# Optimization experiments

Measured on AMD Instinct MI355X. Metric: run time of the kernel, lower is better.

## Reference

```python
import jax, jax.numpy as jnp
import numpy as np

H, W = 256, 256          # heat_map_shape
P = 512                  # number of ground-truth points
ALPHA = -5.0             # soft-min exponent


def setup_inputs() -> dict:
    key = jax.random.key(0)
    k1, k2 = jax.random.split(key)
    heat_map = jax.random.uniform(k1, (H, W), dtype=jnp.float32)  # values in [0,1]
    # points in [0,H) x [0,W), float coords (never exactly on grid -> dist > 0)
    points = jax.random.uniform(k2, (P, 2), dtype=jnp.float32) * jnp.array([H, W], jnp.float32)
    return {"heat_map": heat_map, "points": points}


def reference(heat_map, points):
    # grid: (H, W, 2) with torch.meshgrid 'ij' indexing semantics
    ys = jnp.arange(H, dtype=jnp.float32)
    xs = jnp.arange(W, dtype=jnp.float32)
    grid = jnp.stack(jnp.meshgrid(ys, xs, indexing="ij"), axis=-1)

    delta = grid[:, :, None, :] - points[None, None]          # (H, W, P, 2)
    dist = jnp.sqrt(jnp.sum(delta * delta, axis=-1))          # (H, W, P)

    # term 1: heatmap-weighted min distance, normalized by L1 norm of heatmap
    weighted_min = jnp.sum(heat_map * jnp.min(dist, axis=-1)) / jnp.sum(jnp.abs(heat_map))

    # term 2: generalized (power) mean soft-min over spatial dims, then mean over P
    hm = heat_map[..., None]                                  # (H, W, 1)
    weighted_dist = hm * dist + (1.0 - hm) * jnp.max(dist)    # (H, W, P)
    soft_min = jnp.mean(weighted_dist ** ALPHA, axis=(0, 1)) ** (1.0 / ALPHA)  # (P,)
    mean_soft_min = jnp.mean(soft_min)

    return weighted_min + mean_soft_min
```

## Files before the change

### kernel.cpp

```cpp
#include <hip/hip_runtime.h>

#define HH 256
#define WW 256
#define NPIX (HH * WW)
#define NP 512

#define PPB 4
#define SLICE_ROWS 32
#define NSLICES (HH / SLICE_ROWS)
#define NPGRP (NP / PPB)
#define NB_T2 (NPGRP * NSLICES)
#define NB_T1 (NPIX / 256)
#define NB_TOTAL (NB_T1 + NB_T2)

#define WS_SP   0
#define WS_T1A  (NP * NSLICES)
#define WS_T1B  (WS_T1A + NB_T1)

__global__ __launch_bounds__(256) void whd_main(const float* __restrict__ hm,
                                                const float* __restrict__ pts,
                                                float* __restrict__ ws) {
    const int tid = threadIdx.x;
    const int bid = blockIdx.x;
    __shared__ float sred[PPB][4];
    __shared__ float dred[4];

    if (bid < NB_T1) {
        const int idx = bid * 256 + tid;
        const float fi = (float)(idx >> 8);
        const float fj = (float)(idx & (WW - 1));
        const float4* pts4 = (const float4*)pts;
        float m0 = 3.4e38f, m1 = 3.4e38f, m2 = 3.4e38f, m3 = 3.4e38f;
        #pragma unroll 4
        for (int i = 0; i < NP / 2; i += 4) {
            float4 q0 = pts4[i], q1 = pts4[i + 1], q2 = pts4[i + 2], q3 = pts4[i + 3];
            float dy, dx;
            dy = fi - q0.x; dx = fj - q0.y; m0 = fminf(m0, fmaf(dy, dy, dx * dx));
            dy = fi - q0.z; dx = fj - q0.w; m1 = fminf(m1, fmaf(dy, dy, dx * dx));
            dy = fi - q1.x; dx = fj - q1.y; m2 = fminf(m2, fmaf(dy, dy, dx * dx));
            dy = fi - q1.z; dx = fj - q1.w; m3 = fminf(m3, fmaf(dy, dy, dx * dx));
            dy = fi - q2.x; dx = fj - q2.y; m0 = fminf(m0, fmaf(dy, dy, dx * dx));
            dy = fi - q2.z; dx = fj - q2.w; m1 = fminf(m1, fmaf(dy, dy, dx * dx));
            dy = fi - q3.x; dx = fj - q3.y; m2 = fminf(m2, fmaf(dy, dy, dx * dx));
            dy = fi - q3.z; dx = fj - q3.w; m3 = fminf(m3, fmaf(dy, dy, dx * dx));
        }
        float mind = __builtin_amdgcn_sqrtf(fminf(fminf(m0, m1), fminf(m2, m3)));
        float h  = hm[idx];
        float v1 = h * mind;
        float v2 = fabsf(h);
        #pragma unroll
        for (int off = 32; off; off >>= 1) {
            v1 += __shfl_down(v1, off, 64);
            v2 += __shfl_down(v2, off, 64);
        }
        if ((tid & 63) == 0) { sred[0][tid >> 6] = v1; sred[1][tid >> 6] = v2; }
        __syncthreads();
        if (tid == 0) ws[WS_T1A + bid] = sred[0][0] + sred[0][1] + sred[0][2] + sred[0][3];
        if (tid == 1) ws[WS_T1B + bid] = sred[1][0] + sred[1][1] + sred[1][2] + sred[1][3];
    } else {
        const int b2 = bid - NB_T1;
        float m = 0.f;
        #pragma unroll
        for (int t = 0; t < 2; ++t) {
            int p = tid + t * 256;
            float py = pts[2 * p], px = pts[2 * p + 1];
            float my = fmaxf(py * py, (255.f - py) * (255.f - py));
            float mx = fmaxf(px * px, (255.f - px) * (255.f - px));
            m = fmaxf(m, my + mx);
        }
        #pragma unroll
        for (int off = 32; off; off >>= 1) m = fmaxf(m, __shfl_down(m, off, 64));
        if ((tid & 63) == 0) dred[tid >> 6] = m;
        __syncthreads();
        const float dmax = __builtin_amdgcn_sqrtf(
            fmaxf(fmaxf(dred[0], dred[1]), fmaxf(dred[2], dred[3])));

        const int pgrp  = b2 & (NPGRP - 1);
        const int slice = b2 >> 7;
        const int p0    = pgrp * PPB;

        float py[PPB], px[PPB];
        #pragma unroll
        for (int a = 0; a < PPB; ++a) {
            py[a] = pts[2 * (p0 + a)];
            px[a] = pts[2 * (p0 + a) + 1];
        }

        const float col0 = (float)((tid & 63) << 2);
        float dx2[PPB][4];
        #pragma unroll
        for (int a = 0; a < PPB; ++a)
            #pragma unroll
            for (int c = 0; c < 4; ++c) {
                float dx = col0 + (float)c - px[a];
                dx2[a][c] = dx * dx;
            }

        const float4* hm4 = (const float4*)hm;
        const int   gbase   = slice * (SLICE_ROWS * WW / 4) + tid;
        const float rowbase = (float)(slice * SLICE_ROWS + (tid >> 6));
        float acc[PPB] = {0.f, 0.f, 0.f, 0.f};

        #pragma unroll
        for (int k = 0; k < 8; ++k) {
            float4 h4 = hm4[gbase + k * 256];
            const float row = rowbase + (float)(4 * k);
            const float hx[4] = {h4.x, h4.y, h4.z, h4.w};
            float ct[4];
            #pragma unroll
            for (int c = 0; c < 4; ++c) ct[c] = fmaf(-hx[c], dmax, dmax);
            float dy2[PPB];
            #pragma unroll
            for (int a = 0; a < PPB; ++a) { float dy = row - py[a]; dy2[a] = dy * dy; }

            #pragma unroll
            for (int a = 0; a < PPB; ++a) {
                #pragma unroll
                for (int c = 0; c < 4; ++c) {
                    float d  = __builtin_amdgcn_sqrtf(dy2[a] + dx2[a][c]);
                    float w  = fmaf(hx[c], d, ct[c]);
                    float r  = __builtin_amdgcn_rcpf(w);
                    float r2 = r * r;
                    acc[a]   = fmaf(r2 * r2, r, acc[a]);
                }
            }
        }

        #pragma unroll
        for (int a = 0; a < PPB; ++a) {
            float v = acc[a];
            #pragma unroll
            for (int off = 32; off; off >>= 1) v += __shfl_down(v, off, 64);
            if ((tid & 63) == 0) sred[a][tid >> 6] = v;
        }
        __syncthreads();
        if (tid < PPB) {
            ws[WS_SP + (p0 + tid) * NSLICES + slice] =
                sred[tid][0] + sred[tid][1] + sred[tid][2] + sred[tid][3];
        }
    }
}

__global__ __launch_bounds__(NP) void whd_final(const float* __restrict__ ws,
                                                float* __restrict__ out) {
    const int t = threadIdx.x;
    const float4* w4 = (const float4*)(ws + WS_SP);
    float4 a = w4[t * 2], b = w4[t * 2 + 1];
    float S = ((a.x + a.y) + (a.z + a.w)) + ((b.x + b.y) + (b.z + b.w));
    float sm = exp2f(-0.2f * log2f(S * (1.f / (float)NPIX)));
    float v1 = (t < NB_T1) ? ws[WS_T1A + t] : 0.f;
    float v2 = (t < NB_T1) ? ws[WS_T1B + t] : 0.f;

    #pragma unroll
    for (int off = 32; off; off >>= 1) {
        sm += __shfl_down(sm, off, 64);
        v1 += __shfl_down(v1, off, 64);
        v2 += __shfl_down(v2, off, 64);
    }
    __shared__ float red[3][8];
    if ((t & 63) == 0) { int w = t >> 6; red[0][w] = sm; red[1][w] = v1; red[2][w] = v2; }
    __syncthreads();
    if (t == 0) {
        float rsm = 0.f, r1 = 0.f, r2 = 0.f;
        #pragma unroll
        for (int w = 0; w < 8; ++w) { rsm += red[0][w]; r1 += red[1][w]; r2 += red[2][w]; }
        out[0] = r1 / r2 + rsm * (1.f / (float)NP);
    }
}

extern "C" void kernel_launch(void* const* d_in, const int* in_sizes, int n_in,
                              void* d_out, int out_size, void* d_ws, size_t ws_size,
                              hipStream_t stream) {
    const float* hm  = (const float*)d_in[0];
    const float* pts = (const float*)d_in[1];
    float* ws  = (float*)d_ws;
    float* out = (float*)d_out;

    whd_main <<<NB_TOTAL, 256, 0, stream>>>(hm, pts, ws);
    whd_final<<<1,        NP,  0, stream>>>(ws, out);
}
```

Measured before the change: 70.47 us.

## Restructure distance math into float2 pairs for packed FP32 and prefetch heatmap

Rewrites both the min-distance and soft-min inner loops to work on float2 pairs so the compiler can emit packed FP32 (v_pk_fma/v_pk_mul/v_pk_add) instructions on CDNA. It also loads all eight heatmap float4s into registers up front rather than inside the compute loop, and interleaves the wavefront shuffle reductions across the four points. Sqrt and rcp have no packed form, so the transcendental-heavy soft-min path may gain little, and the extra live registers could reduce occupancy.

```diff
diff --git a/kernel.cpp b/kernel.cpp
--- a/kernel.cpp
+++ b/kernel.cpp
@@ -17,6 +17,23 @@
 #define WS_T1A  (NP * NSLICES)
 #define WS_T1B  (WS_T1A + NB_T1)
 
+__device__ __forceinline__ float2 pk2(float a, float b) { return make_float2(a, b); }
+__device__ __forceinline__ float2 pk_add(float2 a, float2 b) { return make_float2(a.x + b.x, a.y + b.y); }
+__device__ __forceinline__ float2 pk_sub(float2 a, float2 b) { return make_float2(a.x - b.x, a.y - b.y); }
+__device__ __forceinline__ float2 pk_mul(float2 a, float2 b) { return make_float2(a.x * b.x, a.y * b.y); }
+__device__ __forceinline__ float2 pk_fma(float2 a, float2 b, float2 c) {
+    return make_float2(fmaf(a.x, b.x, c.x), fmaf(a.y, b.y, c.y));
+}
+__device__ __forceinline__ float2 pk_min(float2 a, float2 b) {
+    return make_float2(fminf(a.x, b.x), fminf(a.y, b.y));
+}
+__device__ __forceinline__ float2 pk_sqrt(float2 a) {
+    return make_float2(__builtin_amdgcn_sqrtf(a.x), __builtin_amdgcn_sqrtf(a.y));
+}
+__device__ __forceinline__ float2 pk_rcp(float2 a) {
+    return make_float2(__builtin_amdgcn_rcpf(a.x), __builtin_amdgcn_rcpf(a.y));
+}
+
 __global__ __launch_bounds__(256) void whd_main(const float* __restrict__ hm,
                                                 const float* __restrict__ pts,
                                                 float* __restrict__ ws) {
@@ -29,22 +46,24 @@
         const int idx = bid * 256 + tid;
         const float fi = (float)(idx >> 8);
         const float fj = (float)(idx & (WW - 1));
+        const float2 fi2 = pk2(fi, fi), fj2 = pk2(fj, fj);
         const float4* pts4 = (const float4*)pts;
-        float m0 = 3.4e38f, m1 = 3.4e38f, m2 = 3.4e38f, m3 = 3.4e38f;
+        float2 ma = pk2(3.4e38f, 3.4e38f), mb = ma, mc = ma, md = ma;
         #pragma unroll 4
         for (int i = 0; i < NP / 2; i += 4) {
             float4 q0 = pts4[i], q1 = pts4[i + 1], q2 = pts4[i + 2], q3 = pts4[i + 3];
-            float dy, dx;
-            dy = fi - q0.x; dx = fj - q0.y; m0 = fminf(m0, fmaf(dy, dy, dx * dx));
-            dy = fi - q0.z; dx = fj - q0.w; m1 = fminf(m1, fmaf(dy, dy, dx * dx));
-            dy = fi - q1.x; dx = fj - q1.y; m2 = fminf(m2, fmaf(dy, dy, dx * dx));
-            dy = fi - q1.z; dx = fj - q1.w; m3 = fminf(m3, fmaf(dy, dy, dx * dx));
-            dy = fi - q2.x; dx = fj - q2.y; m0 = fminf(m0, fmaf(dy, dy, dx * dx));
-            dy = fi - q2.z; dx = fj - q2.w; m1 = fminf(m1, fmaf(dy, dy, dx * dx));
-            dy = fi - q3.x; dx = fj - q3.y; m2 = fminf(m2, fmaf(dy, dy, dx * dx));
-            dy = fi - q3.z; dx = fj - q3.w; m3 = fminf(m3, fmaf(dy, dy, dx * dx));
-        }
-        float mind = __builtin_amdgcn_sqrtf(fminf(fminf(m0, m1), fminf(m2, m3)));
+            float2 dy, dx;
+            dy = pk_sub(fi2, pk2(q0.x, q0.z)); dx = pk_sub(fj2, pk2(q0.y, q0.w));
+            ma = pk_min(ma, pk_fma(dy, dy, pk_mul(dx, dx)));
+            dy = pk_sub(fi2, pk2(q1.x, q1.z)); dx = pk_sub(fj2, pk2(q1.y, q1.w));
+            mb = pk_min(mb, pk_fma(dy, dy, pk_mul(dx, dx)));
+            dy = pk_sub(fi2, pk2(q2.x, q2.z)); dx = pk_sub(fj2, pk2(q2.y, q2.w));
+            mc = pk_min(mc, pk_fma(dy, dy, pk_mul(dx, dx)));
+            dy = pk_sub(fi2, pk2(q3.x, q3.z)); dx = pk_sub(fj2, pk2(q3.y, q3.w));
+            md = pk_min(md, pk_fma(dy, dy, pk_mul(dx, dx)));
+        }
+        float2 mm = pk_min(pk_min(ma, mb), pk_min(mc, md));
+        float mind = __builtin_amdgcn_sqrtf(fminf(mm.x, mm.y));
         float h  = hm[idx];
         float v1 = h * mind;
         float v2 = fabsf(h);
@@ -74,6 +93,7 @@
         __syncthreads();
         const float dmax = __builtin_amdgcn_sqrtf(
             fmaxf(fmaxf(dred[0], dred[1]), fmaxf(dred[2], dred[3])));
+        const float2 dmax2 = pk2(dmax, dmax);
 
         const int pgrp  = b2 & (NPGRP - 1);
         const int slice = b2 >> 7;
@@ -87,51 +107,64 @@
         }
 
         const float col0 = (float)((tid & 63) << 2);
-        float dx2[PPB][4];
-        #pragma unroll
-        for (int a = 0; a < PPB; ++a)
-            #pragma unroll
-            for (int c = 0; c < 4; ++c) {
-                float dx = col0 + (float)c - px[a];
-                dx2[a][c] = dx * dx;
-            }
+        float2 dx2A[PPB], dx2B[PPB];
+        #pragma unroll
+        for (int a = 0; a < PPB; ++a) {
+            float2 dA = pk2(col0 + 0.f - px[a], col0 + 1.f - px[a]);
+            float2 dB = pk2(col0 + 2.f - px[a], col0 + 3.f - px[a]);
+            dx2A[a] = pk_mul(dA, dA);
+            dx2B[a] = pk_mul(dB, dB);
+        }
 
         const float4* hm4 = (const float4*)hm;
         const int   gbase   = slice * (SLICE_ROWS * WW / 4) + tid;
         const float rowbase = (float)(slice * SLICE_ROWS + (tid >> 6));
-        float acc[PPB] = {0.f, 0.f, 0.f, 0.f};
-
+
+        float4 h4s[8];
+        #pragma unroll
+        for (int k = 0; k < 8; ++k) h4s[k] = hm4[gbase + k * 256];
+
+        float2 accA[PPB], accB[PPB];
+        #pragma unroll
+        for (int a = 0; a < PPB; ++a) { accA[a] = pk2(0.f, 0.f); accB[a] = pk2(0.f, 0.f); }
+
+        const float2 one2 = pk2(1.f, 1.f);
         #pragma unroll
         for (int k = 0; k < 8; ++k) {
-            float4 h4 = hm4[gbase + k * 256];
+            const float4 h4 = h4s[k];
             const float row = rowbase + (float)(4 * k);
-            const float hx[4] = {h4.x, h4.y, h4.z, h4.w};
-            float ct[4];
-            #pragma unroll
-            for (int c = 0; c < 4; ++c) ct[c] = fmaf(-hx[c], dmax, dmax);
-            float dy2[PPB];
-            #pragma unroll
-            for (int a = 0; a < PPB; ++a) { float dy = row - py[a]; dy2[a] = dy * dy; }
+            const float2 hA = pk2(h4.x, h4.y), hB = pk2(h4.z, h4.w);
+            const float2 ctA = pk_mul(pk_sub(one2, hA), dmax2);
+            const float2 ctB = pk_mul(pk_sub(one2, hB), dmax2);
 
             #pragma unroll
             for (int a = 0; a < PPB; ++a) {
-                #pragma unroll
-                for (int c = 0; c < 4; ++c) {
-                    float d  = __builtin_amdgcn_sqrtf(dy2[a] + dx2[a][c]);
-                    float w  = fmaf(hx[c], d, ct[c]);
-                    float r  = __builtin_amdgcn_rcpf(w);
-                    float r2 = r * r;
-                    acc[a]   = fmaf(r2 * r2, r, acc[a]);
-                }
+                float dy = row - py[a];
+                float2 dy2 = pk2(dy * dy, dy * dy);
+                float2 dA = pk_sqrt(pk_add(dy2, dx2A[a]));
+                float2 dB = pk_sqrt(pk_add(dy2, dx2B[a]));
+                float2 wA = pk_fma(hA, dA, ctA);
+                float2 wB = pk_fma(hB, dB, ctB);
+                float2 rA = pk_rcp(wA);
+                float2 rB = pk_rcp(wB);
+                float2 r2A = pk_mul(rA, rA), r2B = pk_mul(rB, rB);
+                accA[a] = pk_fma(pk_mul(r2A, r2A), rA, accA[a]);
+                accB[a] = pk_fma(pk_mul(r2B, r2B), rB, accB[a]);
             }
         }
 
-        #pragma unroll
-        for (int a = 0; a < PPB; ++a) {
-            float v = acc[a];
+        float v[PPB];
+        #pragma unroll
+        for (int a = 0; a < PPB; ++a)
+            v[a] = (accA[a].x + accA[a].y) + (accB[a].x + accB[a].y);
+        #pragma unroll
+        for (int off = 32; off; off >>= 1) {
             #pragma unroll
-            for (int off = 32; off; off >>= 1) v += __shfl_down(v, off, 64);
-            if ((tid & 63) == 0) sred[a][tid >> 6] = v;
+            for (int a = 0; a < PPB; ++a) v[a] += __shfl_down(v[a], off, 64);
+        }
+        if ((tid & 63) == 0) {
+            #pragma unroll
+            for (int a = 0; a < PPB; ++a) sred[a][tid >> 6] = v[a];
         }
         __syncthreads();
         if (tid < PPB) {
```

New measurement: 72.45 us. +2.8%, slower.

## Pack soft-min math into f32x2 ops and batch reciprocals across four pixels

Applied to the files above, without the earlier changes.

Rewrites the term-2 inner loop to use packed FP32 instructions (v_pk_add/mul/fma) for pairs of columns. It replaces four per-pixel reciprocals with one shared reciprocal plus product-based reconstruction (Montgomery batch inversion), cutting transcendental-unit work. It also hoists all heatmap loads ahead of the dmax reduction so they overlap, and computes dmax on a single wavefront. The batched inverse risks overflow or underflow of the four-way product and adds multiplies. Inline asm may also limit compiler scheduling.

```diff
diff --git a/kernel.cpp b/kernel.cpp
--- a/kernel.cpp
+++ b/kernel.cpp
@@ -17,13 +17,24 @@
 #define WS_T1A  (NP * NSLICES)
 #define WS_T1B  (WS_T1A + NB_T1)
 
+typedef float f32x2 __attribute__((ext_vector_type(2)));
+__device__ __forceinline__ f32x2 pk_add(f32x2 a, f32x2 b) {
+    f32x2 d; asm("v_pk_add_f32 %0, %1, %2" : "=v"(d) : "v"(a), "v"(b)); return d;
+}
+__device__ __forceinline__ f32x2 pk_mul(f32x2 a, f32x2 b) {
+    f32x2 d; asm("v_pk_mul_f32 %0, %1, %2" : "=v"(d) : "v"(a), "v"(b)); return d;
+}
+__device__ __forceinline__ f32x2 pk_fma(f32x2 a, f32x2 b, f32x2 c) {
+    f32x2 d; asm("v_pk_fma_f32 %0, %1, %2, %3" : "=v"(d) : "v"(a), "v"(b), "v"(c)); return d;
+}
+
 __global__ __launch_bounds__(256) void whd_main(const float* __restrict__ hm,
                                                 const float* __restrict__ pts,
                                                 float* __restrict__ ws) {
     const int tid = threadIdx.x;
     const int bid = blockIdx.x;
     __shared__ float sred[PPB][4];
-    __shared__ float dred[4];
+    __shared__ float dmax_sh;
 
     if (bid < NB_T1) {
         const int idx = bid * 256 + tid;
@@ -58,27 +69,34 @@
         if (tid == 0) ws[WS_T1A + bid] = sred[0][0] + sred[0][1] + sred[0][2] + sred[0][3];
         if (tid == 1) ws[WS_T1B + bid] = sred[1][0] + sred[1][1] + sred[1][2] + sred[1][3];
     } else {
-        const int b2 = bid - NB_T1;
-        float m = 0.f;
-        #pragma unroll
-        for (int t = 0; t < 2; ++t) {
-            int p = tid + t * 256;
-            float py = pts[2 * p], px = pts[2 * p + 1];
-            float my = fmaxf(py * py, (255.f - py) * (255.f - py));
-            float mx = fmaxf(px * px, (255.f - px) * (255.f - px));
-            m = fmaxf(m, my + mx);
-        }
-        #pragma unroll
-        for (int off = 32; off; off >>= 1) m = fmaxf(m, __shfl_down(m, off, 64));
-        if ((tid & 63) == 0) dred[tid >> 6] = m;
-        __syncthreads();
-        const float dmax = __builtin_amdgcn_sqrtf(
-            fmaxf(fmaxf(dred[0], dred[1]), fmaxf(dred[2], dred[3])));
-
+        const int b2    = bid - NB_T1;
         const int pgrp  = b2 & (NPGRP - 1);
         const int slice = b2 >> 7;
         const int p0    = pgrp * PPB;
 
+        const float4* hm4 = (const float4*)hm;
+        const int gbase = slice * (SLICE_ROWS * WW / 4) + tid;
+        float4 h4s[8];
+        #pragma unroll
+        for (int k = 0; k < 8; ++k) h4s[k] = hm4[gbase + k * 256];
+
+        if (tid < 64) {
+            float m = 0.f;
+            #pragma unroll
+            for (int t = 0; t < 8; ++t) {
+                int p = tid + t * 64;
+                float py_ = pts[2 * p], px_ = pts[2 * p + 1];
+                float my = fmaxf(py_ * py_, (255.f - py_) * (255.f - py_));
+                float mx = fmaxf(px_ * px_, (255.f - px_) * (255.f - px_));
+                m = fmaxf(m, my + mx);
+            }
+            #pragma unroll
+            for (int off = 32; off; off >>= 1) m = fmaxf(m, __shfl_down(m, off, 64));
+            if (tid == 0) dmax_sh = __builtin_amdgcn_sqrtf(m);
+        }
+        __syncthreads();
+        const float dmax = dmax_sh;
+
         float py[PPB], px[PPB];
         #pragma unroll
         for (int a = 0; a < PPB; ++a) {
@@ -87,51 +105,73 @@
         }
 
         const float col0 = (float)((tid & 63) << 2);
-        float dx2[PPB][4];
+        f32x2 dx2A[PPB], dx2B[PPB];
+        #pragma unroll
+        for (int a = 0; a < PPB; ++a) {
+            float d0 = col0 + 0.f - px[a], d1 = col0 + 1.f - px[a];
+            float d2 = col0 + 2.f - px[a], d3 = col0 + 3.f - px[a];
+            dx2A[a].x = d0 * d0; dx2A[a].y = d1 * d1;
+            dx2B[a].x = d2 * d2; dx2B[a].y = d3 * d3;
+        }
+
+        const float rowbase = (float)(slice * SLICE_ROWS + (tid >> 6));
+        f32x2 accA[PPB], accB[PPB];
+        #pragma unroll
+        for (int a = 0; a < PPB; ++a) {
+            accA[a].x = 0.f; accA[a].y = 0.f;
+            accB[a].x = 0.f; accB[a].y = 0.f;
+        }
+
+        #pragma unroll
+        for (int k = 0; k < 8; ++k) {
+            const float4 h4 = h4s[k];
+            const float row = rowbase + (float)(4 * k);
+            f32x2 hA;  hA.x = h4.x;  hA.y = h4.y;
+            f32x2 hB;  hB.x = h4.z;  hB.y = h4.w;
+            f32x2 ctA; ctA.x = fmaf(-h4.x, dmax, dmax); ctA.y = fmaf(-h4.y, dmax, dmax);
+            f32x2 ctB; ctB.x = fmaf(-h4.z, dmax, dmax); ctB.y = fmaf(-h4.w, dmax, dmax);
+
+            #pragma unroll
+            for (int a = 0; a < PPB; ++a) {
+                float dy  = row - py[a];
+                float dy2 = dy * dy;
+                f32x2 dy2p; dy2p.x = dy2; dy2p.y = dy2;
+                f32x2 sA = pk_add(dy2p, dx2A[a]);
+                f32x2 sB = pk_add(dy2p, dx2B[a]);
+                f32x2 dA, dB;
+                dA.x = __builtin_amdgcn_sqrtf(sA.x); dA.y = __builtin_amdgcn_sqrtf(sA.y);
+                dB.x = __builtin_amdgcn_sqrtf(sB.x); dB.y = __builtin_amdgcn_sqrtf(sB.y);
+                f32x2 wA = pk_fma(hA, dA, ctA);
+                f32x2 wB = pk_fma(hB, dB, ctB);
+                float p1 = wA.x * wA.y;
+                float p2 = p1 * wB.x;
+                float p3 = p2 * wB.y;
+                float r  = __builtin_amdgcn_rcpf(p3);
+                float i3 = r * p2;
+                float q  = r * wB.y;
+                float i2 = q * p1;
+                float q2 = q * wB.x;
+                f32x2 iA; iA.x = q2 * wA.y; iA.y = q2 * wA.x;
+                f32x2 iB; iB.x = i2;        iB.y = i3;
+                f32x2 tA = pk_mul(iA, iA);
+                f32x2 tB = pk_mul(iB, iB);
+                accA[a] = pk_fma(pk_mul(tA, tA), iA, accA[a]);
+                accB[a] = pk_fma(pk_mul(tB, tB), iB, accB[a]);
+            }
+        }
+
+        float v[PPB];
         #pragma unroll
         for (int a = 0; a < PPB; ++a)
-            #pragma unroll
-            for (int c = 0; c < 4; ++c) {
-                float dx = col0 + (float)c - px[a];
-                dx2[a][c] = dx * dx;
-            }
-
-        const float4* hm4 = (const float4*)hm;
-        const int   gbase   = slice * (SLICE_ROWS * WW / 4) + tid;
-        const float rowbase = (float)(slice * SLICE_ROWS + (tid >> 6));
-        float acc[PPB] = {0.f, 0.f, 0.f, 0.f};
-
-        #pragma unroll
-        for (int k = 0; k < 8; ++k) {
-            float4 h4 = hm4[gbase + k * 256];
-            const float row = rowbase + (float)(4 * k);
-            const float hx[4] = {h4.x, h4.y, h4.z, h4.w};
-            float ct[4];
-            #pragma unroll
-            for (int c = 0; c < 4; ++c) ct[c] = fmaf(-hx[c], dmax, dmax);
-            float dy2[PPB];
-            #pragma unroll
-            for (int a = 0; a < PPB; ++a) { float dy = row - py[a]; dy2[a] = dy * dy; }
-
-            #pragma unroll
-            for (int a = 0; a < PPB; ++a) {
-                #pragma unroll
-                for (int c = 0; c < 4; ++c) {
-                    float d  = __builtin_amdgcn_sqrtf(dy2[a] + dx2[a][c]);
-                    float w  = fmaf(hx[c], d, ct[c]);
-                    float r  = __builtin_amdgcn_rcpf(w);
-                    float r2 = r * r;
-                    acc[a]   = fmaf(r2 * r2, r, acc[a]);
-                }
-            }
-        }
-
-        #pragma unroll
-        for (int a = 0; a < PPB; ++a) {
-            float v = acc[a];
-            #pragma unroll
-            for (int off = 32; off; off >>= 1) v += __shfl_down(v, off, 64);
-            if ((tid & 63) == 0) sred[a][tid >> 6] = v;
+            v[a] = (accA[a].x + accA[a].y) + (accB[a].x + accB[a].y);
+        #pragma unroll
+        for (int off = 32; off; off >>= 1) {
+            #pragma unroll
+            for (int a = 0; a < PPB; ++a) v[a] += __shfl_down(v[a], off, 64);
+        }
+        if ((tid & 63) == 0) {
+            #pragma unroll
+            for (int a = 0; a < PPB; ++a) sred[a][tid >> 6] = v[a];
         }
         __syncthreads();
         if (tid < PPB) {
```

Result: no change. 70.77 us (+0.4%).
